# Kernel optimization log

Measured on AMD Instinct MI355X. Metric: run time of the kernel, lower is better.

The kernel has to match this reference:

```python
import jax, jax.numpy as jnp
import numpy as np

B, N, CQ, CKV, CP = 4, 1024, 128, 64, 16
H, NB = 4, 3
D = CQ // H  # 32 per-head dim
NQ, NK = 32, 128
CENTRES = 15.5 + 32.0 * np.arange(N // NQ)  # subset centres covering all atoms


def _ln(x, eps=1e-5):
    m = jnp.mean(x, axis=-1, keepdims=True)
    v = jnp.var(x, axis=-1, keepdims=True)
    return (x - m) * jax.lax.rsqrt(v + eps)


def _adaln(a, s, s_gamma, w_gate, w_skip):
    # AF3 AdaLN: a normalized without affine, modulated by conditioning s
    a_n = _ln(a)
    s_n = _ln(s) * s_gamma
    return jax.nn.sigmoid(s_n @ w_gate) * a_n + s_n @ w_skip


def _local_bias():
    # sequence-local block mask (union over subset centres), Algorithm 7
    idx = jnp.arange(N, dtype=jnp.float32)
    cen = jnp.asarray(CENTRES, dtype=jnp.float32)
    lcond = jnp.abs(idx[None, :] - cen[:, None]) < NQ / 2  # [C, N] query window
    mcond = jnp.abs(idx[None, :] - cen[:, None]) < NK / 2  # [C, N] key window
    cond = jnp.any(lcond[:, :, None] & mcond[:, None, :], axis=0)  # [N, N]
    return jnp.where(cond, 0.0, -1e10)


def _forward(q, c, p, attn_s_gamma, attn_gate_w, attn_skip_w, attn_wq, attn_bq,
             attn_wk, attn_wv, attn_lnz_g, attn_lnz_b, attn_wb, attn_wgate,
             attn_wo, attn_ws_out, attn_bs_out, trans_s_gamma, trans_gate_w,
             trans_skip_w, trans_w1, trans_w2, trans_wout, trans_ws_out,
             trans_bs_out):
    beta = _local_bias()  # [N, N]
    inv_sqrt_d = 1.0 / np.sqrt(D)
    a = q
    for i in range(NB):  # 3 structurally distinct blocks
        # --- AttentionPairBias (AF3 Alg 24) ---
        ah = _adaln(a, c, attn_s_gamma[i], attn_gate_w[i], attn_skip_w[i])
        qh = (ah @ attn_wq[i] + attn_bq[i]).reshape(B, N, H, D)
        kh = (ah @ attn_wk[i]).reshape(B, N, H, D)
        vh = (ah @ attn_wv[i]).reshape(B, N, H, D)
        zb = (_ln(p) * attn_lnz_g[i] + attn_lnz_b[i]) @ attn_wb[i]  # [B,N,N,H]
        bias = jnp.transpose(zb, (0, 3, 1, 2)) + beta[None, None]  # [B,H,N,N]
        scores = jnp.einsum('bqhd,bkhd->bhqk', qh, kh) * inv_sqrt_d + bias
        w = jax.nn.softmax(scores, axis=-1)
        o = jnp.einsum('bhqk,bkhd->bqhd', w, vh)
        g = jax.nn.sigmoid((ah @ attn_wgate[i]).reshape(B, N, H, D))
        o = (g * o).reshape(B, N, CQ) @ attn_wo[i]
        attn_out = jax.nn.sigmoid(c @ attn_ws_out[i] + attn_bs_out[i]) * o
        # --- ConditionedTransitionBlock (AF3 Alg 25, n=2 SwiGLU) ---
        t = _adaln(a, c, trans_s_gamma[i], trans_gate_w[i], trans_skip_w[i])
        bm = jax.nn.silu(t @ trans_w1[i]) * (t @ trans_w2[i])
        t_out = jax.nn.sigmoid(c @ trans_ws_out[i] + trans_bs_out[i]) * (bm @ trans_wout[i])
        # AF3 Alg 23: a <- attn_out + transition(a, s)
        a = attn_out + t_out
    return a


def setup_inputs() -> dict:
    key = jax.random.key(0)
    ks = iter(jax.random.split(key, 64))

    def rnd(shape, scale=0.02):
        return jax.random.normal(next(ks), shape, dtype=jnp.float32) * scale

    return {
        'q': jax.random.normal(next(ks), (B, N, CQ), dtype=jnp.float32),
        'c': jax.random.normal(next(ks), (B, N, CKV), dtype=jnp.float32),
        'p': jax.random.normal(next(ks), (B, N, N, CP), dtype=jnp.float32),
        'attn_s_gamma': jnp.ones((NB, CKV), jnp.float32),
        'attn_gate_w': rnd((NB, CKV, CQ)),
        'attn_skip_w': rnd((NB, CKV, CQ)),
        'attn_wq': rnd((NB, CQ, CQ)),
        'attn_bq': jnp.zeros((NB, CQ), jnp.float32),
        'attn_wk': rnd((NB, CQ, CQ)),
        'attn_wv': rnd((NB, CQ, CQ)),
        'attn_lnz_g': jnp.ones((NB, CP), jnp.float32),
        'attn_lnz_b': jnp.zeros((NB, CP), jnp.float32),
        'attn_wb': rnd((NB, CP, H)),
        'attn_wgate': rnd((NB, CQ, CQ)),
        'attn_wo': rnd((NB, CQ, CQ)),
        'attn_ws_out': rnd((NB, CKV, CQ)),
        'attn_bs_out': jnp.full((NB, CQ), -2.0, jnp.float32),
        'trans_s_gamma': jnp.ones((NB, CKV), jnp.float32),
        'trans_gate_w': rnd((NB, CKV, CQ)),
        'trans_skip_w': rnd((NB, CKV, CQ)),
        'trans_w1': rnd((NB, CQ, 2 * CQ)),
        'trans_w2': rnd((NB, CQ, 2 * CQ)),
        'trans_wout': rnd((NB, 2 * CQ, CQ)),
        'trans_ws_out': rnd((NB, CKV, CQ)),
        'trans_bs_out': jnp.full((NB, CQ), -2.0, jnp.float32),
    }


def reference(q, c, p, attn_s_gamma, attn_gate_w, attn_skip_w, attn_wq, attn_bq,
              attn_wk, attn_wv, attn_lnz_g, attn_lnz_b, attn_wb, attn_wgate,
              attn_wo, attn_ws_out, attn_bs_out, trans_s_gamma, trans_gate_w,
              trans_skip_w, trans_w1, trans_w2, trans_wout, trans_ws_out,
              trans_bs_out):
    return _forward(q, c, p, attn_s_gamma, attn_gate_w, attn_skip_w, attn_wq,
                    attn_bq, attn_wk, attn_wv, attn_lnz_g, attn_lnz_b, attn_wb,
                    attn_wgate, attn_wo, attn_ws_out, attn_bs_out,
                    trans_s_gamma, trans_gate_w, trans_skip_w, trans_w1,
                    trans_w2, trans_wout, trans_ws_out, trans_bs_out)
```

## Files before the change

### kernel.cpp

```cpp
#include <hip/hip_runtime.h>
#include <math.h>

#define NB_ 3
#define B_ 4
#define N_ 1024
#define CQ_ 128
#define CKV_ 64
#define CP_ 16
#define H_ 4
#define D_ 32
#define R_ (B_*N_)
#define KW_ 128

__device__ __forceinline__ float sigmoidf_(float x) {
    return 1.0f / (1.0f + __expf(-x));
}

#define AN_OFF 0
#define SA_OFF 1056
#define ST_OFF 1600
#define CR_OFF 2144
#define TH_OFF 2688
#define SCR_OFF 3744
#define SMEM_F (3744 + 6336)

__global__ __launch_bounds__(512, 4) void k_pre(
    const float* __restrict__ a, const float* __restrict__ c,
    const float* __restrict__ a_sg, const float* __restrict__ a_gw,
    const float* __restrict__ a_sw, const float* __restrict__ a_wso,
    const float* __restrict__ a_bso,
    const float* __restrict__ t_sg, const float* __restrict__ t_gw,
    const float* __restrict__ t_sw, const float* __restrict__ t_wso,
    const float* __restrict__ t_bso,
    const float* __restrict__ wq, const float* __restrict__ bq,
    const float* __restrict__ wk, const float* __restrict__ wv,
    const float* __restrict__ wg,
    const float* __restrict__ w1, const float* __restrict__ w2,
    float* __restrict__ qh, float* __restrict__ kh,
    float* __restrict__ vh, float* __restrict__ gh,
    float* __restrict__ bm,
    float* __restrict__ asig, float* __restrict__ tsig)
{
    __shared__ float smem[SMEM_F];
    const int t = threadIdx.x;
    const int base = blockIdx.x * 8;

    {
        const int rloc = t >> 6, li = t & 63;
        const int row = base + rloc;
        float2 av = *(const float2*)(a + row * 128 + li * 2);
        float s = av.x + av.y;
        float ss = av.x * av.x + av.y * av.y;
        float cv = c[row * 64 + li];
        float cs = cv, css = cv * cv;
        #pragma unroll
        for (int m = 1; m < 64; m <<= 1) {
            s += __shfl_xor(s, m);
            ss += __shfl_xor(ss, m);
            cs += __shfl_xor(cs, m);
            css += __shfl_xor(css, m);
        }
        const float am = s * (1.0f / 128.0f);
        const float ars = rsqrtf(ss * (1.0f / 128.0f) - am * am + 1e-5f);
        const float cm = cs * (1.0f / 64.0f);
        const float crs = rsqrtf(css * (1.0f / 64.0f) - cm * cm + 1e-5f);
        smem[AN_OFF + rloc * 132 + li * 2]     = (av.x - am) * ars;
        smem[AN_OFF + rloc * 132 + li * 2 + 1] = (av.y - am) * ars;
        const float cn = (cv - cm) * crs;
        smem[SA_OFF + rloc * 68 + li] = cn * a_sg[li];
        smem[ST_OFF + rloc * 68 + li] = cn * t_sg[li];
        smem[CR_OFF + rloc * 68 + li] = cv;
    }
    __syncthreads();

    const int wave = t >> 6;
    const int lane = t & 63;
    const int ig = lane >> 4;
    const int jc = lane & 15;
    const int c0 = jc * 8;
    const int r0 = ig * 2, r1 = ig * 2 + 1;

    if (wave < 6) {
        const float* W;
        const float* xs;
        switch (wave) {
            case 0: W = a_gw;  xs = smem + SA_OFF; break;
            case 1: W = a_sw;  xs = smem + SA_OFF; break;
            case 2: W = t_gw;  xs = smem + ST_OFF; break;
            case 3: W = t_sw;  xs = smem + ST_OFF; break;
            case 4: W = a_wso; xs = smem + CR_OFF; break;
            default: W = t_wso; xs = smem + CR_OFF; break;
        }
        W += c0;
        float acc0[8], acc1[8];
        #pragma unroll
        for (int e = 0; e < 8; e++) { acc0[e] = 0.f; acc1[e] = 0.f; }
        for (int kk = 0; kk < 64; kk += 4) {
            float4 x40 = *(const float4*)(xs + r0 * 68 + kk);
            float4 x41 = *(const float4*)(xs + r1 * 68 + kk);
            #pragma unroll
            for (int q = 0; q < 4; q++) {
                const float4 wlo = *(const float4*)(W + (kk + q) * 128);
                const float4 whi = *(const float4*)(W + (kk + q) * 128 + 4);
                const float xa = ((const float*)&x40)[q];
                const float xb = ((const float*)&x41)[q];
                acc0[0] += xa * wlo.x; acc0[1] += xa * wlo.y;
                acc0[2] += xa * wlo.z; acc0[3] += xa * wlo.w;
                acc0[4] += xa * whi.x; acc0[5] += xa * whi.y;
                acc0[6] += xa * whi.z; acc0[7] += xa * whi.w;
                acc1[0] += xb * wlo.x; acc1[1] += xb * wlo.y;
                acc1[2] += xb * wlo.z; acc1[3] += xb * wlo.w;
                acc1[4] += xb * whi.x; acc1[5] += xb * whi.y;
                acc1[6] += xb * whi.z; acc1[7] += xb * whi.w;
            }
        }
        float* sc = smem + SCR_OFF + wave * 1056;
        *(float4*)(sc + r0 * 132 + c0)     = make_float4(acc0[0], acc0[1], acc0[2], acc0[3]);
        *(float4*)(sc + r0 * 132 + c0 + 4) = make_float4(acc0[4], acc0[5], acc0[6], acc0[7]);
        *(float4*)(sc + r1 * 132 + c0)     = make_float4(acc1[0], acc1[1], acc1[2], acc1[3]);
        *(float4*)(sc + r1 * 132 + c0 + 4) = make_float4(acc1[4], acc1[5], acc1[6], acc1[7]);
    }
    __syncthreads();

    #pragma unroll
    for (int i2 = 0; i2 < 2; i2++) {
        const int e = t + i2 * 512;
        const int r = e >> 7, cc = e & 127;
        const float* sc = smem + SCR_OFF + r * 132 + cc;
        const float anv = smem[AN_OFF + r * 132 + cc];
        const float ahv = sigmoidf_(sc[0]) * anv + sc[1056];
        const float thv = sigmoidf_(sc[2 * 1056]) * anv + sc[3 * 1056];
        smem[AN_OFF + r * 132 + cc] = ahv;
        smem[TH_OFF + r * 132 + cc] = thv;
        const int idx = (base + r) * 128 + cc;
        asig[idx] = sigmoidf_(sc[4 * 1056] + a_bso[cc]);
        tsig[idx] = sigmoidf_(sc[5 * 1056] + t_bso[cc]);
    }
    __syncthreads();

    {
        const float* W;
        const float* xs;
        int ldw, sel2 = 0, cb = 0;
        if (wave < 4) {
            W = (wave == 0 ? wq : wave == 1 ? wk : wave == 2 ? wv : wg) + c0;
            xs = smem + AN_OFF;
            ldw = 128;
        } else {
            const int u = (wave - 4) * 128 + c0;
            sel2 = u >> 8; cb = u & 255;
            W = (sel2 ? w2 : w1) + cb;
            xs = smem + TH_OFF;
            ldw = 256;
        }
        float acc0[8], acc1[8];
        #pragma unroll
        for (int e = 0; e < 8; e++) {
            const float init = (wave == 0) ? bq[c0 + e] : 0.f;
            acc0[e] = init; acc1[e] = init;
        }
        for (int kk = 0; kk < 128; kk += 4) {
            float4 x40 = *(const float4*)(xs + r0 * 132 + kk);
            float4 x41 = *(const float4*)(xs + r1 * 132 + kk);
            #pragma unroll
            for (int q = 0; q < 4; q++) {
                const float4 wlo = *(const float4*)(W + (kk + q) * ldw);
                const float4 whi = *(const float4*)(W + (kk + q) * ldw + 4);
                const float xa = ((const float*)&x40)[q];
                const float xb = ((const float*)&x41)[q];
                acc0[0] += xa * wlo.x; acc0[1] += xa * wlo.y;
                acc0[2] += xa * wlo.z; acc0[3] += xa * wlo.w;
                acc0[4] += xa * whi.x; acc0[5] += xa * whi.y;
                acc0[6] += xa * whi.z; acc0[7] += xa * whi.w;
                acc1[0] += xb * wlo.x; acc1[1] += xb * wlo.y;
                acc1[2] += xb * wlo.z; acc1[3] += xb * wlo.w;
                acc1[4] += xb * whi.x; acc1[5] += xb * whi.y;
                acc1[6] += xb * whi.z; acc1[7] += xb * whi.w;
            }
        }
        if (wave < 4) {
            float* dst = (wave == 0 ? qh : wave == 1 ? kh : wave == 2 ? vh : gh);
            if (wave == 3) {
                #pragma unroll
                for (int e = 0; e < 8; e++) {
                    acc0[e] = sigmoidf_(acc0[e]);
                    acc1[e] = sigmoidf_(acc1[e]);
                }
            }
            *(float4*)(dst + (base + r0) * 128 + c0)     = make_float4(acc0[0], acc0[1], acc0[2], acc0[3]);
            *(float4*)(dst + (base + r0) * 128 + c0 + 4) = make_float4(acc0[4], acc0[5], acc0[6], acc0[7]);
            *(float4*)(dst + (base + r1) * 128 + c0)     = make_float4(acc1[0], acc1[1], acc1[2], acc1[3]);
            *(float4*)(dst + (base + r1) * 128 + c0 + 4) = make_float4(acc1[4], acc1[5], acc1[6], acc1[7]);
        } else {
            float* bsc = smem + SCR_OFF + sel2 * 2080;
            *(float4*)(bsc + r0 * 260 + cb)     = make_float4(acc0[0], acc0[1], acc0[2], acc0[3]);
            *(float4*)(bsc + r0 * 260 + cb + 4) = make_float4(acc0[4], acc0[5], acc0[6], acc0[7]);
            *(float4*)(bsc + r1 * 260 + cb)     = make_float4(acc1[0], acc1[1], acc1[2], acc1[3]);
            *(float4*)(bsc + r1 * 260 + cb + 4) = make_float4(acc1[4], acc1[5], acc1[6], acc1[7]);
        }
    }
    __syncthreads();

    #pragma unroll
    for (int i2 = 0; i2 < 4; i2++) {
        const int e = t + i2 * 512;
        const int r = e >> 8, cc = e & 255;
        const float a1 = smem[SCR_OFF + r * 260 + cc];
        const float a2 = smem[SCR_OFF + 2080 + r * 260 + cc];
        bm[(base + r) * 256 + cc] = a1 * sigmoidf_(a1) * a2;
    }
}

__global__ __launch_bounds__(256) void k_zbias(
    const float* __restrict__ p,
    const float* __restrict__ lnz_g, const float* __restrict__ lnz_b,
    const float* __restrict__ wb, float* __restrict__ zb)
{
    const int tid = blockIdx.x * 256 + threadIdx.x;
    const int kk = tid & 127;
    const int n = (tid >> 7) & 1023;
    const int b = tid >> 17;
    const int row = b * N_ + n;
    const int k = ((n >> 5) << 5) - 48 + kk;

    if (k < 0 || k >= N_) {
        #pragma unroll
        for (int blk = 0; blk < NB_; blk++) {
            float* zo = zb + ((size_t)(blk * R_ + row) * H_) * KW_ + kk;
            #pragma unroll
            for (int h = 0; h < H_; h++) zo[h * KW_] = -1e10f;
        }
        return;
    }
    const float* pp = p + ((size_t)row * N_ + k) * CP_;
    float pv[16];
    float4 p0 = *(const float4*)(pp);
    float4 p1 = *(const float4*)(pp + 4);
    float4 p2 = *(const float4*)(pp + 8);
    float4 p3 = *(const float4*)(pp + 12);
    pv[0]=p0.x; pv[1]=p0.y; pv[2]=p0.z; pv[3]=p0.w;
    pv[4]=p1.x; pv[5]=p1.y; pv[6]=p1.z; pv[7]=p1.w;
    pv[8]=p2.x; pv[9]=p2.y; pv[10]=p2.z; pv[11]=p2.w;
    pv[12]=p3.x; pv[13]=p3.y; pv[14]=p3.z; pv[15]=p3.w;
    float s = 0.f, ss = 0.f;
    #pragma unroll
    for (int i = 0; i < 16; i++) { s += pv[i]; ss += pv[i] * pv[i]; }
    const float m = s * (1.0f / 16.0f);
    const float rs = rsqrtf(ss * (1.0f / 16.0f) - m * m + 1e-5f);

    #pragma unroll
    for (int blk = 0; blk < NB_; blk++) {
        const float* g = lnz_g + blk * 16;
        const float* bb = lnz_b + blk * 16;
        const float* w = wb + blk * 64;
        float z0 = 0.f, z1 = 0.f, z2 = 0.f, z3 = 0.f;
        #pragma unroll
        for (int cp = 0; cp < 16; cp++) {
            const float val = (pv[cp] - m) * rs * g[cp] + bb[cp];
            z0 += val * w[cp * 4 + 0];
            z1 += val * w[cp * 4 + 1];
            z2 += val * w[cp * 4 + 2];
            z3 += val * w[cp * 4 + 3];
        }
        float* zo = zb + ((size_t)(blk * R_ + row) * H_) * KW_ + kk;
        zo[0] = z0; zo[KW_] = z1; zo[2 * KW_] = z2; zo[3 * KW_] = z3;
    }
}

__global__ __launch_bounds__(256) void k_attn(
    const float* __restrict__ qh, const float* __restrict__ kh,
    const float* __restrict__ vh, const float* __restrict__ gh,
    const float* __restrict__ zb, float* __restrict__ og)
{
    __shared__ float kT[32][136];
    __shared__ float vs[128][36];
    __shared__ float wsm[32][132];

    const int t = threadIdx.x;
    const int qb = blockIdx.x, h = blockIdx.y, b = blockIdx.z;
    const int k0 = qb * 32 - 48;

    #pragma unroll
    for (int i = 0; i < 16; i++) {
        const int e = t + i * 256;
        const int kk = e >> 5, d = e & 31;
        const int kg = k0 + kk;
        float kvv = 0.f, vvv = 0.f;
        if (kg >= 0 && kg < N_) {
            const int addr = (b * N_ + kg) * 128 + h * 32 + d;
            kvv = kh[addr]; vvv = vh[addr];
        }
        kT[d][kk] = kvv;
        vs[kk][d] = vvv;
    }

    const int q = t >> 3, j = t & 7;
    const int n = qb * 32 + q;
    const float* qrow = qh + (b * N_ + n) * 128 + h * 32;
    float4 qf[8];
    #pragma unroll
    for (int dq = 0; dq < 8; dq++) qf[dq] = *(const float4*)(qrow + dq * 4);
    const float* zrow = zb + ((size_t)(b * N_ + n) * H_ + h) * KW_;
    float4 zf[4];
    #pragma unroll
    for (int g4 = 0; g4 < 4; g4++) zf[g4] = *(const float4*)(zrow + j * 16 + g4 * 4);
    __syncthreads();

    float4 acc[4];
    #pragma unroll
    for (int g4 = 0; g4 < 4; g4++) acc[g4] = make_float4(0.f, 0.f, 0.f, 0.f);
    const float* qfs = (const float*)qf;
    for (int d = 0; d < 32; d++) {
        const float qd = qfs[d];
        #pragma unroll
        for (int g4 = 0; g4 < 4; g4++) {
            const float4 k4 = *(const float4*)&kT[d][j * 16 + g4 * 4];
            acc[g4].x += qd * k4.x; acc[g4].y += qd * k4.y;
            acc[g4].z += qd * k4.z; acc[g4].w += qd * k4.w;
        }
    }
    const float scale = 0.1767766952966369f;
    float fr[16];
    #pragma unroll
    for (int g4 = 0; g4 < 4; g4++) {
        fr[g4*4+0] = zf[g4].x + acc[g4].x * scale;
        fr[g4*4+1] = zf[g4].y + acc[g4].y * scale;
        fr[g4*4+2] = zf[g4].z + acc[g4].z * scale;
        fr[g4*4+3] = zf[g4].w + acc[g4].w * scale;
    }
    float mx = fr[0];
    #pragma unroll
    for (int i = 1; i < 16; i++) mx = fmaxf(mx, fr[i]);
    #pragma unroll
    for (int mk = 1; mk < 8; mk <<= 1) mx = fmaxf(mx, __shfl_xor(mx, mk));
    float sum = 0.f;
    #pragma unroll
    for (int i = 0; i < 16; i++) { fr[i] = __expf(fr[i] - mx); sum += fr[i]; }
    #pragma unroll
    for (int mk = 1; mk < 8; mk <<= 1) sum += __shfl_xor(sum, mk);
    const float rinv = 1.0f / sum;
    #pragma unroll
    for (int g4 = 0; g4 < 4; g4++)
        #pragma unroll
        for (int mm = 0; mm < 4; mm++)
            wsm[q][j * 16 + g4 * 4 + mm] = fr[g4 * 4 + mm] * rinv;
    __syncthreads();

    const int q2 = t >> 3, dg = t & 7;
    float4 o = make_float4(0.f, 0.f, 0.f, 0.f);
    for (int kk = 0; kk < 128; kk++) {
        const float wv_ = wsm[q2][kk];
        const float4 v4 = *(const float4*)&vs[kk][dg * 4];
        o.x += wv_ * v4.x; o.y += wv_ * v4.y;
        o.z += wv_ * v4.z; o.w += wv_ * v4.w;
    }
    const int n2 = qb * 32 + q2;
    const int addr = (b * N_ + n2) * 128 + h * 32 + dg * 4;
    const float4 g4v = *(const float4*)(gh + addr);
    float4 outv;
    outv.x = o.x * g4v.x; outv.y = o.y * g4v.y;
    outv.z = o.z * g4v.z; outv.w = o.w * g4v.w;
    *(float4*)(og + addr) = outv;
}

__global__ __launch_bounds__(256, 4) void k_combine(
    const float* __restrict__ og, const float* __restrict__ bm,
    const float* __restrict__ wo, const float* __restrict__ wout,
    const float* __restrict__ asig, const float* __restrict__ tsig,
    float* __restrict__ out)
{
    __shared__ float scr[4 * 1056];
    const int t = threadIdx.x;
    const int base = blockIdx.x * 8;
    const int wave = t >> 6, lane = t & 63;
    const int ig = lane >> 4, jc = lane & 15;
    const int c0 = jc * 8;
    const int r0 = ig * 2, r1 = ig * 2 + 1;

    float acc0[8], acc1[8];
    #pragma unroll
    for (int e = 0; e < 8; e++) { acc0[e] = 0.f; acc1[e] = 0.f; }

    if (wave < 2) {
        const float* W = wo + c0;
        const float* X = og + base * 128;
        const int kbeg = wave * 64;
        for (int kk = kbeg; kk < kbeg + 64; kk += 4) {
            float4 x40 = *(const float4*)(X + r0 * 128 + kk);
            float4 x41 = *(const float4*)(X + r1 * 128 + kk);
            #pragma unroll
            for (int q = 0; q < 4; q++) {
                const float4 wlo = *(const float4*)(W + (kk + q) * 128);
                const float4 whi = *(const float4*)(W + (kk + q) * 128 + 4);
                const float xa = ((const float*)&x40)[q];
                const float xb = ((const float*)&x41)[q];
                acc0[0] += xa * wlo.x; acc0[1] += xa * wlo.y;
                acc0[2] += xa * wlo.z; acc0[3] += xa * wlo.w;
                acc0[4] += xa * whi.x; acc0[5] += xa * whi.y;
                acc0[6] += xa * whi.z; acc0[7] += xa * whi.w;
                acc1[0] += xb * wlo.x; acc1[1] += xb * wlo.y;
                acc1[2] += xb * wlo.z; acc1[3] += xb * wlo.w;
                acc1[4] += xb * whi.x; acc1[5] += xb * whi.y;
                acc1[6] += xb * whi.z; acc1[7] += xb * whi.w;
            }
        }
    } else {
        const float* W = wout + c0;
        const float* X = bm + base * 256;
        const int kbeg = (wave - 2) * 128;
        for (int kk = kbeg; kk < kbeg + 128; kk += 4) {
            float4 x40 = *(const float4*)(X + r0 * 256 + kk);
            float4 x41 = *(const float4*)(X + r1 * 256 + kk);
            #pragma unroll
            for (int q = 0; q < 4; q++) {
                const float4 wlo = *(const float4*)(W + (kk + q) * 128);
                const float4 whi = *(const float4*)(W + (kk + q) * 128 + 4);
                const float xa = ((const float*)&x40)[q];
                const float xb = ((const float*)&x41)[q];
                acc0[0] += xa * wlo.x; acc0[1] += xa * wlo.y;
                acc0[2] += xa * wlo.z; acc0[3] += xa * wlo.w;
                acc0[4] += xa * whi.x; acc0[5] += xa * whi.y;
                acc0[6] += xa * whi.z; acc0[7] += xa * whi.w;
                acc1[0] += xb * wlo.x; acc1[1] += xb * wlo.y;
                acc1[2] += xb * wlo.z; acc1[3] += xb * wlo.w;
                acc1[4] += xb * whi.x; acc1[5] += xb * whi.y;
                acc1[6] += xb * whi.z; acc1[7] += xb * whi.w;
            }
        }
    }
    float* sc = scr + wave * 1056;
    *(float4*)(sc + r0 * 132 + c0)     = make_float4(acc0[0], acc0[1], acc0[2], acc0[3]);
    *(float4*)(sc + r0 * 132 + c0 + 4) = make_float4(acc0[4], acc0[5], acc0[6], acc0[7]);
    *(float4*)(sc + r1 * 132 + c0)     = make_float4(acc1[0], acc1[1], acc1[2], acc1[3]);
    *(float4*)(sc + r1 * 132 + c0 + 4) = make_float4(acc1[4], acc1[5], acc1[6], acc1[7]);
    __syncthreads();

    #pragma unroll
    for (int i2 = 0; i2 < 4; i2++) {
        const int e = t + i2 * 256;
        const int r = e >> 7, cc = e & 127;
        const float* s = scr + r * 132 + cc;
        const int idx = (base + r) * 128 + cc;
        out[idx] = asig[idx] * (s[0] + s[1056]) + tsig[idx] * (s[2112] + s[3168]);
    }
}

extern "C" void kernel_launch(void* const* d_in, const int* in_sizes, int n_in,
                              void* d_out, int out_size, void* d_ws, size_t ws_size,
                              hipStream_t stream)
{
    const float* q        = (const float*)d_in[0];
    const float* c        = (const float*)d_in[1];
    const float* p        = (const float*)d_in[2];
    const float* a_sg_all = (const float*)d_in[3];
    const float* a_gw_all = (const float*)d_in[4];
    const float* a_sw_all = (const float*)d_in[5];
    const float* wq_all   = (const float*)d_in[6];
    const float* bq_all   = (const float*)d_in[7];
    const float* wk_all   = (const float*)d_in[8];
    const float* wv_all   = (const float*)d_in[9];
    const float* lnzg_all = (const float*)d_in[10];
    const float* lnzb_all = (const float*)d_in[11];
    const float* wb_all   = (const float*)d_in[12];
    const float* wgt_all  = (const float*)d_in[13];
    const float* wo_all   = (const float*)d_in[14];
    const float* awso_all = (const float*)d_in[15];
    const float* abso_all = (const float*)d_in[16];
    const float* t_sg_all = (const float*)d_in[17];
    const float* t_gw_all = (const float*)d_in[18];
    const float* t_sw_all = (const float*)d_in[19];
    const float* w1_all   = (const float*)d_in[20];
    const float* w2_all   = (const float*)d_in[21];
    const float* wout_all = (const float*)d_in[22];
    const float* twso_all = (const float*)d_in[23];
    const float* tbso_all = (const float*)d_in[24];

    float* ws = (float*)d_ws;
    const size_t RC = (size_t)R_ * CQ_;
    float* qh   = ws;
    float* kh   = ws + RC;
    float* vh   = ws + 2 * RC;
    float* gh   = ws + 3 * RC;
    float* bmb  = ws + 4 * RC;
    float* asig = ws + 6 * RC;
    float* tsig = ws + 7 * RC;
    float* abuf = ws + 8 * RC;
    float* ogb  = ws + 9 * RC;
    float* zbb  = ws + 10 * RC;

    k_zbias<<<dim3(B_ * N_ * KW_ / 256), dim3(256), 0, stream>>>(
        p, lnzg_all, lnzb_all, wb_all, zbb);

    const float* acur = q;
    for (int blk = 0; blk < NB_; blk++) {
        k_pre<<<dim3(R_ / 8), dim3(512), 0, stream>>>(
            acur, c,
            a_sg_all + blk * CKV_, a_gw_all + blk * CKV_ * CQ_,
            a_sw_all + blk * CKV_ * CQ_, awso_all + blk * CKV_ * CQ_,
            abso_all + blk * CQ_,
            t_sg_all + blk * CKV_, t_gw_all + blk * CKV_ * CQ_,
            t_sw_all + blk * CKV_ * CQ_, twso_all + blk * CKV_ * CQ_,
            tbso_all + blk * CQ_,
            wq_all + blk * CQ_ * CQ_, bq_all + blk * CQ_,
            wk_all + blk * CQ_ * CQ_, wv_all + blk * CQ_ * CQ_,
            wgt_all + blk * CQ_ * CQ_,
            w1_all + blk * CQ_ * 2 * CQ_, w2_all + blk * CQ_ * 2 * CQ_,
            qh, kh, vh, gh, bmb, asig, tsig);
        k_attn<<<dim3(N_ / 32, H_, B_), dim3(256), 0, stream>>>(
            qh, kh, vh, gh, zbb + (size_t)blk * R_ * H_ * KW_, ogb);
        float* outp = (blk == NB_ - 1) ? (float*)d_out : abuf;
        k_combine<<<dim3(R_ / 8), dim3(256), 0, stream>>>(
            ogb, bmb, wo_all + blk * CQ_ * CQ_, wout_all + blk * 2 * CQ_ * CQ_,
            asig, tsig, outp);
        acur = abuf;
    }
}
```

Baseline: 646.5 us.

## Hoist conditioning projections into one batched kernel and vectorize attention loads

The AdaLN gate/skip and output-gate projections of c depend only on the conditioning input, not on the evolving activations. They are moved out of the per-block k_pre into a single k_cond launch covering all three blocks, and their results are stored in workspace. k_pre then only normalises a and combines it with the precomputed gate and skip tensors. k_attn switches to float4 K/V staging, interleaved column mapping to cut LDS bank conflicts, and a per-thread PV loop without a barrier. Extra unroll pragmas and launch bounds are added, and the workspace grows by 18 RC buffers of extra global traffic.

```diff
diff --git a/kernel.cpp b/kernel.cpp
--- a/kernel.cpp
+++ b/kernel.cpp
@@ -11,37 +11,130 @@
 #define D_ 32
 #define R_ (B_*N_)
 #define KW_ 128
+#define RC_ (R_*CQ_)
 
 __device__ __forceinline__ float sigmoidf_(float x) {
     return 1.0f / (1.0f + __expf(-x));
 }
 
-#define AN_OFF 0
-#define SA_OFF 1056
-#define ST_OFF 1600
-#define CR_OFF 2144
-#define TH_OFF 2688
-#define SCR_OFF 3744
-#define SMEM_F (3744 + 6336)
-
-__global__ __launch_bounds__(512, 4) void k_pre(
-    const float* __restrict__ a, const float* __restrict__ c,
+__global__ __launch_bounds__(512, 4) void k_cond(
+    const float* __restrict__ c,
     const float* __restrict__ a_sg, const float* __restrict__ a_gw,
     const float* __restrict__ a_sw, const float* __restrict__ a_wso,
     const float* __restrict__ a_bso,
     const float* __restrict__ t_sg, const float* __restrict__ t_gw,
     const float* __restrict__ t_sw, const float* __restrict__ t_wso,
     const float* __restrict__ t_bso,
+    float* __restrict__ gA, float* __restrict__ kA,
+    float* __restrict__ gT, float* __restrict__ kT2,
+    float* __restrict__ asig, float* __restrict__ tsig)
+{
+    __shared__ float xs_s[3 * 544];
+    const int t = threadIdx.x;
+    const int blk = blockIdx.y;
+    const int base = blockIdx.x * 8;
+
+    {
+        const int rloc = t >> 6, li = t & 63;
+        const int row = base + rloc;
+        const float cv = c[row * 64 + li];
+        float cs = cv, css = cv * cv;
+        #pragma unroll
+        for (int m = 1; m < 64; m <<= 1) {
+            cs += __shfl_xor(cs, m);
+            css += __shfl_xor(css, m);
+        }
+        const float cm = cs * (1.0f / 64.0f);
+        const float crs = rsqrtf(css * (1.0f / 64.0f) - cm * cm + 1e-5f);
+        const float cn = (cv - cm) * crs;
+        xs_s[rloc * 68 + li]         = cn * a_sg[blk * 64 + li];
+        xs_s[544 + rloc * 68 + li]   = cn * t_sg[blk * 64 + li];
+        xs_s[1088 + rloc * 68 + li]  = cv;
+    }
+    __syncthreads();
+
+    const int wave = t >> 6, lane = t & 63;
+    if (wave >= 6) return;
+    const int ig = lane >> 4, jc = lane & 15;
+    const int c0 = jc * 8;
+    const int r0 = ig * 2, r1 = r0 + 1;
+
+    const float* W; const float* xs; float* out;
+    int dosig; const float* bias = nullptr;
+    switch (wave) {
+        case 0: W = a_gw;  xs = xs_s;        out = gA;   dosig = 1; break;
+        case 1: W = a_sw;  xs = xs_s;        out = kA;   dosig = 0; break;
+        case 2: W = t_gw;  xs = xs_s + 544;  out = gT;   dosig = 1; break;
+        case 3: W = t_sw;  xs = xs_s + 544;  out = kT2;  dosig = 0; break;
+        case 4: W = a_wso; xs = xs_s + 1088; out = asig; dosig = 1; bias = a_bso; break;
+        default: W = t_wso; xs = xs_s + 1088; out = tsig; dosig = 1; bias = t_bso; break;
+    }
+    W += blk * (CKV_ * CQ_) + c0;
+    out += (size_t)blk * RC_;
+
+    float acc0[8], acc1[8];
+    #pragma unroll
+    for (int e = 0; e < 8; e++) { acc0[e] = 0.f; acc1[e] = 0.f; }
+    #pragma unroll 2
+    for (int kk = 0; kk < 64; kk += 4) {
+        float4 x40 = *(const float4*)(xs + r0 * 68 + kk);
+        float4 x41 = *(const float4*)(xs + r1 * 68 + kk);
+        #pragma unroll
+        for (int q = 0; q < 4; q++) {
+            const float4 wlo = *(const float4*)(W + (kk + q) * 128);
+            const float4 whi = *(const float4*)(W + (kk + q) * 128 + 4);
+            const float xa = ((const float*)&x40)[q];
+            const float xb = ((const float*)&x41)[q];
+            acc0[0] += xa * wlo.x; acc0[1] += xa * wlo.y;
+            acc0[2] += xa * wlo.z; acc0[3] += xa * wlo.w;
+            acc0[4] += xa * whi.x; acc0[5] += xa * whi.y;
+            acc0[6] += xa * whi.z; acc0[7] += xa * whi.w;
+            acc1[0] += xb * wlo.x; acc1[1] += xb * wlo.y;
+            acc1[2] += xb * wlo.z; acc1[3] += xb * wlo.w;
+            acc1[4] += xb * whi.x; acc1[5] += xb * whi.y;
+            acc1[6] += xb * whi.z; acc1[7] += xb * whi.w;
+        }
+    }
+    if (bias) {
+        #pragma unroll
+        for (int e = 0; e < 8; e++) {
+            const float bv = bias[blk * 128 + c0 + e];
+            acc0[e] += bv; acc1[e] += bv;
+        }
+    }
+    if (dosig) {
+        #pragma unroll
+        for (int e = 0; e < 8; e++) {
+            acc0[e] = sigmoidf_(acc0[e]);
+            acc1[e] = sigmoidf_(acc1[e]);
+        }
+    }
+    float* o0 = out + (size_t)(base + r0) * 128 + c0;
+    float* o1 = out + (size_t)(base + r1) * 128 + c0;
+    *(float4*)(o0)     = make_float4(acc0[0], acc0[1], acc0[2], acc0[3]);
+    *(float4*)(o0 + 4) = make_float4(acc0[4], acc0[5], acc0[6], acc0[7]);
+    *(float4*)(o1)     = make_float4(acc1[0], acc1[1], acc1[2], acc1[3]);
+    *(float4*)(o1 + 4) = make_float4(acc1[4], acc1[5], acc1[6], acc1[7]);
+}
+
+#define P_AN 0
+#define P_TH 1056
+#define P_SCR 2112
+#define P_SMEM (2112 + 4160)
+
+__global__ __launch_bounds__(512, 4) void k_pre(
+    const float* __restrict__ a,
+    const float* __restrict__ gA, const float* __restrict__ kA,
+    const float* __restrict__ gT, const float* __restrict__ kT2,
     const float* __restrict__ wq, const float* __restrict__ bq,
     const float* __restrict__ wk, const float* __restrict__ wv,
     const float* __restrict__ wg,
     const float* __restrict__ w1, const float* __restrict__ w2,
     float* __restrict__ qh, float* __restrict__ kh,
     float* __restrict__ vh, float* __restrict__ gh,
-    float* __restrict__ bm,
-    float* __restrict__ asig, float* __restrict__ tsig)
+    float* __restrict__ bm)
 {
-    __shared__ float smem[SMEM_F];
+    __shared__ float smem[P_SMEM];
     const int t = threadIdx.x;
     const int base = blockIdx.x * 8;
 
@@ -51,25 +144,26 @@
         float2 av = *(const float2*)(a + row * 128 + li * 2);
         float s = av.x + av.y;
         float ss = av.x * av.x + av.y * av.y;
-        float cv = c[row * 64 + li];
-        float cs = cv, css = cv * cv;
         #pragma unroll
         for (int m = 1; m < 64; m <<= 1) {
             s += __shfl_xor(s, m);
             ss += __shfl_xor(ss, m);
-            cs += __shfl_xor(cs, m);
-            css += __shfl_xor(css, m);
         }
         const float am = s * (1.0f / 128.0f);
         const float ars = rsqrtf(ss * (1.0f / 128.0f) - am * am + 1e-5f);
-        const float cm = cs * (1.0f / 64.0f);
-        const float crs = rsqrtf(css * (1.0f / 64.0f) - cm * cm + 1e-5f);
-        smem[AN_OFF + rloc * 132 + li * 2]     = (av.x - am) * ars;
-        smem[AN_OFF + rloc * 132 + li * 2 + 1] = (av.y - am) * ars;
-        const float cn = (cv - cm) * crs;
-        smem[SA_OFF + rloc * 68 + li] = cn * a_sg[li];
-        smem[ST_OFF + rloc * 68 + li] = cn * t_sg[li];
-        smem[CR_OFF + rloc * 68 + li] = cv;
+        smem[P_AN + rloc * 132 + li * 2]     = (av.x - am) * ars;
+        smem[P_AN + rloc * 132 + li * 2 + 1] = (av.y - am) * ars;
+    }
+    __syncthreads();
+
+    #pragma unroll
+    for (int i2 = 0; i2 < 2; i2++) {
+        const int e = t + i2 * 512;
+        const int r = e >> 7, cc = e & 127;
+        const int idx = (base + r) * 128 + cc;
+        const float an = smem[P_AN + r * 132 + cc];
+        smem[P_AN + r * 132 + cc] = gA[idx] * an + kA[idx];
+        smem[P_TH + r * 132 + cc] = gT[idx] * an + kT2[idx];
     }
     __syncthreads();
 
@@ -80,77 +174,19 @@
     const int c0 = jc * 8;
     const int r0 = ig * 2, r1 = ig * 2 + 1;
 
-    if (wave < 6) {
-        const float* W;
-        const float* xs;
-        switch (wave) {
-            case 0: W = a_gw;  xs = smem + SA_OFF; break;
-            case 1: W = a_sw;  xs = smem + SA_OFF; break;
-            case 2: W = t_gw;  xs = smem + ST_OFF; break;
-            case 3: W = t_sw;  xs = smem + ST_OFF; break;
-            case 4: W = a_wso; xs = smem + CR_OFF; break;
-            default: W = t_wso; xs = smem + CR_OFF; break;
-        }
-        W += c0;
-        float acc0[8], acc1[8];
-        #pragma unroll
-        for (int e = 0; e < 8; e++) { acc0[e] = 0.f; acc1[e] = 0.f; }
-        for (int kk = 0; kk < 64; kk += 4) {
-            float4 x40 = *(const float4*)(xs + r0 * 68 + kk);
-            float4 x41 = *(const float4*)(xs + r1 * 68 + kk);
-            #pragma unroll
-            for (int q = 0; q < 4; q++) {
-                const float4 wlo = *(const float4*)(W + (kk + q) * 128);
-                const float4 whi = *(const float4*)(W + (kk + q) * 128 + 4);
-                const float xa = ((const float*)&x40)[q];
-                const float xb = ((const float*)&x41)[q];
-                acc0[0] += xa * wlo.x; acc0[1] += xa * wlo.y;
-                acc0[2] += xa * wlo.z; acc0[3] += xa * wlo.w;
-                acc0[4] += xa * whi.x; acc0[5] += xa * whi.y;
-                acc0[6] += xa * whi.z; acc0[7] += xa * whi.w;
-                acc1[0] += xb * wlo.x; acc1[1] += xb * wlo.y;
-                acc1[2] += xb * wlo.z; acc1[3] += xb * wlo.w;
-                acc1[4] += xb * whi.x; acc1[5] += xb * whi.y;
-                acc1[6] += xb * whi.z; acc1[7] += xb * whi.w;
-            }
-        }
-        float* sc = smem + SCR_OFF + wave * 1056;
-        *(float4*)(sc + r0 * 132 + c0)     = make_float4(acc0[0], acc0[1], acc0[2], acc0[3]);
-        *(float4*)(sc + r0 * 132 + c0 + 4) = make_float4(acc0[4], acc0[5], acc0[6], acc0[7]);
-        *(float4*)(sc + r1 * 132 + c0)     = make_float4(acc1[0], acc1[1], acc1[2], acc1[3]);
-        *(float4*)(sc + r1 * 132 + c0 + 4) = make_float4(acc1[4], acc1[5], acc1[6], acc1[7]);
-    }
-    __syncthreads();
-
-    #pragma unroll
-    for (int i2 = 0; i2 < 2; i2++) {
-        const int e = t + i2 * 512;
-        const int r = e >> 7, cc = e & 127;
-        const float* sc = smem + SCR_OFF + r * 132 + cc;
-        const float anv = smem[AN_OFF + r * 132 + cc];
-        const float ahv = sigmoidf_(sc[0]) * anv + sc[1056];
-        const float thv = sigmoidf_(sc[2 * 1056]) * anv + sc[3 * 1056];
-        smem[AN_OFF + r * 132 + cc] = ahv;
-        smem[TH_OFF + r * 132 + cc] = thv;
-        const int idx = (base + r) * 128 + cc;
-        asig[idx] = sigmoidf_(sc[4 * 1056] + a_bso[cc]);
-        tsig[idx] = sigmoidf_(sc[5 * 1056] + t_bso[cc]);
-    }
-    __syncthreads();
-
     {
         const float* W;
         const float* xs;
         int ldw, sel2 = 0, cb = 0;
         if (wave < 4) {
             W = (wave == 0 ? wq : wave == 1 ? wk : wave == 2 ? wv : wg) + c0;
-            xs = smem + AN_OFF;
+            xs = smem + P_AN;
             ldw = 128;
         } else {
             const int u = (wave - 4) * 128 + c0;
             sel2 = u >> 8; cb = u & 255;
             W = (sel2 ? w2 : w1) + cb;
-            xs = smem + TH_OFF;
+            xs = smem + P_TH;
             ldw = 256;
         }
         float acc0[8], acc1[8];
@@ -159,6 +195,7 @@
             const float init = (wave == 0) ? bq[c0 + e] : 0.f;
             acc0[e] = init; acc1[e] = init;
         }
+        #pragma unroll 2
         for (int kk = 0; kk < 128; kk += 4) {
             float4 x40 = *(const float4*)(xs + r0 * 132 + kk);
             float4 x41 = *(const float4*)(xs + r1 * 132 + kk);
@@ -192,7 +229,7 @@
             *(float4*)(dst + (base + r1) * 128 + c0)     = make_float4(acc1[0], acc1[1], acc1[2], acc1[3]);
             *(float4*)(dst + (base + r1) * 128 + c0 + 4) = make_float4(acc1[4], acc1[5], acc1[6], acc1[7]);
         } else {
-            float* bsc = smem + SCR_OFF + sel2 * 2080;
+            float* bsc = smem + P_SCR + sel2 * 2080;
             *(float4*)(bsc + r0 * 260 + cb)     = make_float4(acc0[0], acc0[1], acc0[2], acc0[3]);
             *(float4*)(bsc + r0 * 260 + cb + 4) = make_float4(acc0[4], acc0[5], acc0[6], acc0[7]);
             *(float4*)(bsc + r1 * 260 + cb)     = make_float4(acc1[0], acc1[1], acc1[2], acc1[3]);
@@ -205,8 +242,8 @@
     for (int i2 = 0; i2 < 4; i2++) {
         const int e = t + i2 * 512;
         const int r = e >> 8, cc = e & 255;
-        const float a1 = smem[SCR_OFF + r * 260 + cc];
-        const float a2 = smem[SCR_OFF + 2080 + r * 260 + cc];
+        const float a1 = smem[P_SCR + r * 260 + cc];
+        const float a2 = smem[P_SCR + 2080 + r * 260 + cc];
         bm[(base + r) * 256 + cc] = a1 * sigmoidf_(a1) * a2;
     }
 }
@@ -267,7 +304,7 @@
     }
 }
 
-__global__ __launch_bounds__(256) void k_attn(
+__global__ __launch_bounds__(256, 2) void k_attn(
     const float* __restrict__ qh, const float* __restrict__ kh,
     const float* __restrict__ vh, const float* __restrict__ gh,
     const float* __restrict__ zb, float* __restrict__ og)
@@ -281,17 +318,22 @@
     const int k0 = qb * 32 - 48;
 
     #pragma unroll
-    for (int i = 0; i < 16; i++) {
+    for (int i = 0; i < 4; i++) {
         const int e = t + i * 256;
-        const int kk = e >> 5, d = e & 31;
+        const int kk = e >> 3, d4 = (e & 7) * 4;
         const int kg = k0 + kk;
-        float kvv = 0.f, vvv = 0.f;
+        float4 kv = make_float4(0.f, 0.f, 0.f, 0.f);
+        float4 vv = make_float4(0.f, 0.f, 0.f, 0.f);
         if (kg >= 0 && kg < N_) {
-            const int addr = (b * N_ + kg) * 128 + h * 32 + d;
-            kvv = kh[addr]; vvv = vh[addr];
-        }
-        kT[d][kk] = kvv;
-        vs[kk][d] = vvv;
+            const int addr = (b * N_ + kg) * 128 + h * 32 + d4;
+            kv = *(const float4*)(kh + addr);
+            vv = *(const float4*)(vh + addr);
+        }
+        kT[d4 + 0][kk] = kv.x;
+        kT[d4 + 1][kk] = kv.y;
+        kT[d4 + 2][kk] = kv.z;
+        kT[d4 + 3][kk] = kv.w;
+        *(float4*)&vs[kk][d4] = vv;
     }
 
     const int q = t >> 3, j = t & 7;
@@ -303,18 +345,19 @@
     const float* zrow = zb + ((size_t)(b * N_ + n) * H_ + h) * KW_;
     float4 zf[4];
     #pragma unroll
-    for (int g4 = 0; g4 < 4; g4++) zf[g4] = *(const float4*)(zrow + j * 16 + g4 * 4);
+    for (int g4 = 0; g4 < 4; g4++) zf[g4] = *(const float4*)(zrow + g4 * 32 + j * 4);
     __syncthreads();
 
     float4 acc[4];
     #pragma unroll
     for (int g4 = 0; g4 < 4; g4++) acc[g4] = make_float4(0.f, 0.f, 0.f, 0.f);
     const float* qfs = (const float*)qf;
+    #pragma unroll
     for (int d = 0; d < 32; d++) {
         const float qd = qfs[d];
         #pragma unroll
         for (int g4 = 0; g4 < 4; g4++) {
-            const float4 k4 = *(const float4*)&kT[d][j * 16 + g4 * 4];
+            const float4 k4 = *(const float4*)&kT[d][g4 * 32 + j * 4];
             acc[g4].x += qd * k4.x; acc[g4].y += qd * k4.y;
             acc[g4].z += qd * k4.z; acc[g4].w += qd * k4.w;
         }
@@ -340,27 +383,32 @@
     for (int mk = 1; mk < 8; mk <<= 1) sum += __shfl_xor(sum, mk);
     const float rinv = 1.0f / sum;
     #pragma unroll
-    for (int g4 = 0; g4 < 4; g4++)
-        #pragma unroll
-        for (int mm = 0; mm < 4; mm++)
-            wsm[q][j * 16 + g4 * 4 + mm] = fr[g4 * 4 + mm] * rinv;
-    __syncthreads();
-
-    const int q2 = t >> 3, dg = t & 7;
+    for (int g4 = 0; g4 < 4; g4++) {
+        *(float4*)&wsm[q][g4 * 32 + j * 4] = make_float4(
+            fr[g4*4+0] * rinv, fr[g4*4+1] * rinv,
+            fr[g4*4+2] * rinv, fr[g4*4+3] * rinv);
+    }
+    asm volatile("s_waitcnt lgkmcnt(0)" ::: "memory");
+
+    const int addrO = (b * N_ + n) * 128 + h * 32 + j * 4;
+    const float4 g4v = *(const float4*)(gh + addrO);
     float4 o = make_float4(0.f, 0.f, 0.f, 0.f);
-    for (int kk = 0; kk < 128; kk++) {
-        const float wv_ = wsm[q2][kk];
-        const float4 v4 = *(const float4*)&vs[kk][dg * 4];
-        o.x += wv_ * v4.x; o.y += wv_ * v4.y;
-        o.z += wv_ * v4.z; o.w += wv_ * v4.w;
-    }
-    const int n2 = qb * 32 + q2;
-    const int addr = (b * N_ + n2) * 128 + h * 32 + dg * 4;
-    const float4 g4v = *(const float4*)(gh + addr);
+    #pragma unroll 4
+    for (int kk = 0; kk < 128; kk += 4) {
+        const float4 w4 = *(const float4*)&wsm[q][kk];
+        const float4 v0 = *(const float4*)&vs[kk + 0][j * 4];
+        const float4 v1 = *(const float4*)&vs[kk + 1][j * 4];
+        const float4 v2 = *(const float4*)&vs[kk + 2][j * 4];
+        const float4 v3 = *(const float4*)&vs[kk + 3][j * 4];
+        o.x += w4.x * v0.x + w4.y * v1.x + w4.z * v2.x + w4.w * v3.x;
+        o.y += w4.x * v0.y + w4.y * v1.y + w4.z * v2.y + w4.w * v3.y;
+        o.z += w4.x * v0.z + w4.y * v1.z + w4.z * v2.z + w4.w * v3.z;
+        o.w += w4.x * v0.w + w4.y * v1.w + w4.z * v2.w + w4.w * v3.w;
+    }
     float4 outv;
     outv.x = o.x * g4v.x; outv.y = o.y * g4v.y;
     outv.z = o.z * g4v.z; outv.w = o.w * g4v.w;
-    *(float4*)(og + addr) = outv;
+    *(float4*)(og + addrO) = outv;
 }
 
 __global__ __launch_bounds__(256, 4) void k_combine(
@@ -385,6 +433,7 @@
         const float* W = wo + c0;
         const float* X = og + base * 128;
         const int kbeg = wave * 64;
+        #pragma unroll 2
         for (int kk = kbeg; kk < kbeg + 64; kk += 4) {
             float4 x40 = *(const float4*)(X + r0 * 128 + kk);
             float4 x41 = *(const float4*)(X + r1 * 128 + kk);
@@ -408,6 +457,7 @@
         const float* W = wout + c0;
         const float* X = bm + base * 256;
         const int kbeg = (wave - 2) * 128;
+        #pragma unroll 2
         for (int kk = kbeg; kk < kbeg + 128; kk += 4) {
             float4 x40 = *(const float4*)(X + r0 * 256 + kk);
             float4 x41 = *(const float4*)(X + r1 * 256 + kk);
@@ -476,42 +526,47 @@
     const float* tbso_all = (const float*)d_in[24];
 
     float* ws = (float*)d_ws;
-    const size_t RC = (size_t)R_ * CQ_;
-    float* qh   = ws;
-    float* kh   = ws + RC;
-    float* vh   = ws + 2 * RC;
-    float* gh   = ws + 3 * RC;
-    float* bmb  = ws + 4 * RC;
-    float* asig = ws + 6 * RC;
-    float* tsig = ws + 7 * RC;
-    float* abuf = ws + 8 * RC;
-    float* ogb  = ws + 9 * RC;
-    float* zbb  = ws + 10 * RC;
+    const size_t RC = (size_t)RC_;
+    float* qh    = ws;
+    float* kh    = ws + RC;
+    float* vh    = ws + 2 * RC;
+    float* gh    = ws + 3 * RC;
+    float* bmb   = ws + 4 * RC;
+    float* ogb   = ws + 6 * RC;
+    float* abuf  = ws + 7 * RC;
+    float* zbb   = ws + 8 * RC;
+    float* gAb   = ws + 20 * RC;
+    float* kAb   = ws + 23 * RC;
+    float* gTb   = ws + 26 * RC;
+    float* kT2b  = ws + 29 * RC;
+    float* asigb = ws + 32 * RC;
+    float* tsigb = ws + 35 * RC;
 
     k_zbias<<<dim3(B_ * N_ * KW_ / 256), dim3(256), 0, stream>>>(
         p, lnzg_all, lnzb_all, wb_all, zbb);
+
+    k_cond<<<dim3(R_ / 8, NB_), dim3(512), 0, stream>>>(
+        c, a_sg_all, a_gw_all, a_sw_all, awso_all, abso_all,
+        t_sg_all, t_gw_all, t_sw_all, twso_all, tbso_all,
+        gAb, kAb, gTb, kT2b, asigb, tsigb);
 
     const float* acur = q;
     for (int blk = 0; blk < NB_; blk++) {
         k_pre<<<dim3(R_ / 8), dim3(512), 0, stream>>>(
-            acur, c,
-            a_sg_all + blk * CKV_, a_gw_all + blk * CKV_ * CQ_,
-            a_sw_all + blk * CKV_ * CQ_, awso_all + blk * CKV_ * CQ_,
-            abso_all + blk * CQ_,
-            t_sg_all + blk * CKV_, t_gw_all + blk * CKV_ * CQ_,
-            t_sw_all + blk * CKV_ * CQ_, twso_all + blk * CKV_ * CQ_,
-            tbso_all + blk * CQ_,
+            acur,
+            gAb + (size_t)blk * RC, kAb + (size_t)blk * RC,
+            gTb + (size_t)blk * RC, kT2b + (size_t)blk * RC,
             wq_all + blk * CQ_ * CQ_, bq_all + blk * CQ_,
             wk_all + blk * CQ_ * CQ_, wv_all + blk * CQ_ * CQ_,
             wgt_all + blk * CQ_ * CQ_,
             w1_all + blk * CQ_ * 2 * CQ_, w2_all + blk * CQ_ * 2 * CQ_,
-            qh, kh, vh, gh, bmb, asig, tsig);
+            qh, kh, vh, gh, bmb);
         k_attn<<<dim3(N_ / 32, H_, B_), dim3(256), 0, stream>>>(
             qh, kh, vh, gh, zbb + (size_t)blk * R_ * H_ * KW_, ogb);
         float* outp = (blk == NB_ - 1) ? (float*)d_out : abuf;
         k_combine<<<dim3(R_ / 8), dim3(256), 0, stream>>>(
             ogb, bmb, wo_all + blk * CQ_ * CQ_, wout_all + blk * 2 * CQ_ * CQ_,
-            asig, tsig, outp);
+            asigb + (size_t)blk * RC, tsigb + (size_t)blk * RC, outp);
         acur = abuf;
     }
 }
```

New measurement: 734.4 us. +13.6%, slower.
